# Kernel optimization log

Hardware: AMD Instinct MI355X
Metric: run time of the kernel (lower is better)

The kernel has to match this reference:

```python
import jax, jax.numpy as jnp
import numpy as np

N = 65536          # total nodes across batch
C = 256            # in channels
COUT = 256         # out channels
B = 8              # batch size (graphs)
EMB = 512          # emb channels
N_EDGE_TYPE = 7
N_NODE_TYPE = 7
AVG_DEGREE = 7
E = N * AVG_DEGREE
GROUP = 32         # min(32, channels)
EPS = 1e-5


def setup_inputs() -> dict:
    key = jax.random.key(0)
    ks = jax.random.split(key, 10)
    # GraphConv init: uniform xavier-like with fan scaled by avg_degree
    std = (2.0 / float(AVG_DEGREE * C + AVG_DEGREE * COUT)) ** 0.5
    a = (3.0 ** 0.5) * std
    return {
        "x": jax.random.normal(ks[0], (N, C), jnp.float32),
        "emb": jax.random.normal(ks[1], (B, EMB), jnp.float32),
        "batch_id": jnp.sort(jax.random.randint(ks[2], (N,), 0, B, jnp.int32)),
        "edge_index": jax.random.randint(ks[3], (2, E), 0, N, jnp.int32),
        "edge_type": jax.random.randint(ks[4], (E,), 0, N_EDGE_TYPE, jnp.int32),
        "node_type": jax.random.randint(ks[5], (N,), 0, N_NODE_TYPE, jnp.int32),
        "gn1_w": jnp.ones((1, C), jnp.float32),
        "gn1_b": jnp.zeros((1, C), jnp.float32),
        "conv1_w": jax.random.uniform(ks[6], (N_EDGE_TYPE * (C + N_NODE_TYPE), COUT), jnp.float32, -a, a),
        "emb_w": jax.random.normal(ks[7], (EMB, COUT), jnp.float32) * 0.02,
        "emb_b": jnp.zeros((COUT,), jnp.float32),
        "gn2_w": jnp.ones((1, COUT), jnp.float32),
        "gn2_b": jnp.zeros((1, COUT), jnp.float32),
        "conv2_w": jax.random.uniform(ks[8], (N_EDGE_TYPE * (COUT + N_NODE_TYPE), COUT), jnp.float32, -a, a),
    }


def _adjust_for_group(t, cpg):
    # sum stats within each group of cpg channels, broadcast back: [B, C]
    if cpg > 1:
        Bsz, Cn = t.shape
        g = Cn // cpg
        t = t.reshape(Bsz, g, cpg).sum(-1, keepdims=True)
        t = jnp.broadcast_to(t, (Bsz, g, cpg)).reshape(Bsz, Cn)
    return t


def dual_octree_group_norm(data, batch_id, w, b):
    # data: [N, C]; per-graph group norm via segment sums
    Cn = data.shape[1]
    cpg = Cn // GROUP
    ones = jnp.ones((data.shape[0], 1), data.dtype)
    count = jax.ops.segment_sum(ones, batch_id, num_segments=B) * cpg   # [B,1]
    inv_count = 1.0 / (count + EPS)
    mean = jax.ops.segment_sum(data, batch_id, num_segments=B) * inv_count
    mean = _adjust_for_group(mean, cpg)
    out = data - mean[batch_id]
    var = jax.ops.segment_sum(out * out, batch_id, num_segments=B) * inv_count
    var = _adjust_for_group(var, cpg)
    inv_std = 1.0 / jnp.sqrt(var + EPS)
    out = out * inv_std[batch_id]
    return out * w + b


def graph_conv(x, weights, edge_index, edge_type, node_type):
    # concat one-hot node type channels
    one_hot = jax.nn.one_hot(node_type, N_NODE_TYPE, dtype=x.dtype)
    xa = jnp.concatenate([x, one_hot], axis=1)          # [N, C+T]
    row, col = edge_index[0], edge_index[1]
    index = row * N_EDGE_TYPE + edge_type               # [E]
    col_data = jax.ops.segment_sum(xa[col], index, num_segments=xa.shape[0] * N_EDGE_TYPE)
    return col_data.reshape(xa.shape[0], -1) @ weights  # [N, COUT]


def reference(x, emb, batch_id, edge_index, edge_type, node_type,
              gn1_w, gn1_b, conv1_w, emb_w, emb_b, gn2_w, gn2_b, conv2_w):
    h = dual_octree_group_norm(x, batch_id, gn1_w, gn1_b)
    h = jax.nn.silu(h)
    h = graph_conv(h, conv1_w, edge_index, edge_type, node_type)
    emb_out = jax.nn.silu(emb) @ emb_w + emb_b          # [B, COUT]
    h = h + emb_out[batch_id]                           # per-batch add (loop in torch)
    h = dual_octree_group_norm(h, batch_id, gn2_w, gn2_b)
    h = jax.nn.silu(h)                                  # dropout p=0 -> identity
    h = graph_conv(h, conv2_w, edge_index, edge_type, node_type)
    return x + h                                        # skip is Identity (Cout==C)
```

## Files before the change

### kernel.cpp

```cpp
#include <hip/hip_runtime.h>
#include <math.h>

#define N_NODES 65536
#define B_GR    8
#define EMB_N   512
#define E_EDGES 458752
#define NSEG    458752
#define TSTRIDE 288
#define GK      2016
#define EPS     1e-5f

typedef unsigned short u16;
typedef unsigned int   u32;
typedef __bf16 bf16x8 __attribute__((ext_vector_type(8)));
typedef float  f32x4  __attribute__((ext_vector_type(4)));
typedef u16    u16x8  __attribute__((ext_vector_type(8)));

__device__ __forceinline__ float bf2f(u16 u) {
    u32 x = ((u32)u) << 16; float f; __builtin_memcpy(&f, &x, 4); return f;
}
__device__ __forceinline__ u16 f2bf(float f) {
    u32 x; __builtin_memcpy(&x, &f, 4);
    u32 r = x + 0x7fffu + ((x >> 16) & 1u);
    return (u16)(r >> 16);
}

#define SW(row, k8) ((k8) ^ (((row) >> 1) & 3))

__global__ __launch_bounds__(256) void zero_kernel(int* __restrict__ hist,
                                                   float* __restrict__ S, float* __restrict__ Q,
                                                   int* __restrict__ cnt) {
    int i = blockIdx.x * 256 + threadIdx.x;
    if (i < NSEG) hist[i] = 0;
    if (i < 2048) { S[i] = 0.f; Q[i] = 0.f; }
    if (i < 8) cnt[i] = 0;
}

__global__ __launch_bounds__(256) void count_kernel(const int* __restrict__ batch_id,
                                                    int* __restrict__ cnt) {
    int i = blockIdx.x * 256 + threadIdx.x;
    int b = batch_id[i];
#pragma unroll
    for (int bb = 0; bb < 8; bb++) {
        unsigned long long m = __ballot(b == bb);
        if ((threadIdx.x & 63) == 0 && m)
            atomicAdd(&cnt[bb], (int)__popcll(m));
    }
}

__global__ __launch_bounds__(256) void prep_kernel(
    const float* __restrict__ w1, const float* __restrict__ w2,
    u16* __restrict__ Wt1, u16* __restrict__ Wt2,
    const float* __restrict__ emb, const float* __restrict__ embw,
    const float* __restrict__ embb, float* __restrict__ embout)
{
    int bid = blockIdx.x, tid = threadIdx.x;
    if (bid < 1008) {
        const float* Win = (bid < 504) ? w1 : w2;
        u16* Wt = (bid < 504) ? Wt1 : Wt2;
        int r  = bid % 504;
        int t  = r / 72;
        int r2 = r % 72;
        int c0 = (r2 / 8) * 32;
        int n0 = (r2 % 8) * 32;
        __shared__ float tile[32][33];
        int cl = tid & 31, rh = tid >> 5;
#pragma unroll
        for (int rr = 0; rr < 4; rr++) {
            int c = c0 + rh + rr * 8;
            float v = 0.f;
            if (c < 263) v = Win[(size_t)(t * 263 + c) * 256 + n0 + cl];
            tile[rh + rr * 8][cl] = v;
        }
        __syncthreads();
#pragma unroll
        for (int rr = 0; rr < 4; rr++) {
            int n = n0 + rh + rr * 8;
            Wt[(size_t)n * GK + t * TSTRIDE + c0 + cl] = f2bf(tile[cl][rh + rr * 8]);
        }
    } else {
        __shared__ float semb[B_GR * EMB_N];
        for (int i = tid; i < B_GR * EMB_N; i += 256) {
            float e = emb[i];
            semb[i] = e / (1.f + expf(-e));
        }
        __syncthreads();
        float acc[8];
        float bb = embb[tid];
#pragma unroll
        for (int b = 0; b < 8; b++) acc[b] = bb;
        for (int k = 0; k < EMB_N; k++) {
            float wv = embw[k * 256 + tid];
#pragma unroll
            for (int b = 0; b < 8; b++) acc[b] += semb[b * EMB_N + k] * wv;
        }
#pragma unroll
        for (int b = 0; b < 8; b++) embout[b * 256 + tid] = acc[b];
    }
}

__global__ __launch_bounds__(256) void stats_kernel(const float* __restrict__ xin,
                                                    const int* __restrict__ batch_id,
                                                    float* __restrict__ S, float* __restrict__ Q) {
    int c = threadIdx.x;
    int n0 = blockIdx.x * 64;
    float s = 0.f, q = 0.f;
    int bcur = batch_id[n0];
    for (int r = 0; r < 64; r++) {
        int n = n0 + r;
        int b = batch_id[n];
        if (b != bcur) {
            atomicAdd(&S[bcur * 256 + c], s);
            atomicAdd(&Q[bcur * 256 + c], q);
            s = 0.f; q = 0.f; bcur = b;
        }
        float v = xin[(size_t)n * 256 + c];
        s += v;
        q = fmaf(v, v, q);
    }
    atomicAdd(&S[bcur * 256 + c], s);
    atomicAdd(&Q[bcur * 256 + c], q);
}

__global__ __launch_bounds__(256) void finalize_kernel(const int* __restrict__ cnt,
                                                       float* __restrict__ S, float* __restrict__ Q,
                                                       float* __restrict__ gmean, float* __restrict__ gistd) {
    int tid = threadIdx.x;
    int b = tid >> 5, g = tid & 31;
    float Sg = 0.f, Qg = 0.f;
#pragma unroll
    for (int k = 0; k < 8; k++) {
        int idx = b * 256 + g * 8 + k;
        Sg += S[idx];
        Qg += Q[idx];
        S[idx] = 0.f;
        Q[idx] = 0.f;
    }
    float cnt8 = (float)cnt[b] * 8.f;
    float D = cnt8 + EPS;
    float m = Sg / D;
    float var = (Qg - 2.f * m * Sg + cnt8 * m * m) / D;
    float istd = rsqrtf(var + EPS);
    gmean[tid] = m;
    gistd[tid] = istd;
}

__global__ __launch_bounds__(256) void norm_silu_kernel(const float* __restrict__ xin,
                                                        const int* __restrict__ batch_id,
                                                        const float* __restrict__ gmean, const float* __restrict__ gistd,
                                                        const float* __restrict__ w, const float* __restrict__ bias,
                                                        u16* __restrict__ yout) {
    int tid = threadIdx.x;
    int n = blockIdx.x * 8 + (tid >> 5);
    int g = tid & 31;
    int c0 = g * 8;
    int b = batch_id[n];
    float m = gmean[b * 32 + g], is = gistd[b * 32 + g];
    u16x8 o;
#pragma unroll
    for (int k = 0; k < 8; k++) {
        float v = (xin[(size_t)n * 256 + c0 + k] - m) * is;
        v = v * w[c0 + k] + bias[c0 + k];
        v = v / (1.f + expf(-v));
        o[k] = f2bf(v);
    }
    *(u16x8*)&yout[(size_t)n * 256 + c0] = o;
}

__global__ __launch_bounds__(256) void hist_kernel(const int* __restrict__ ei, const int* __restrict__ et,
                                                   int* __restrict__ hist) {
    int e = blockIdx.x * 256 + threadIdx.x;
    if (e >= E_EDGES) return;
    int s = ei[e] * 7 + et[e];
    atomicAdd(&hist[s], 1);
}

__global__ __launch_bounds__(512) void scan1_kernel(const int* __restrict__ hist, int* __restrict__ partials) {
    __shared__ int sd[512];
    int i = blockIdx.x * 512 + threadIdx.x;
    sd[threadIdx.x] = hist[i];
    __syncthreads();
    for (int off = 256; off > 0; off >>= 1) {
        if (threadIdx.x < off) sd[threadIdx.x] += sd[threadIdx.x + off];
        __syncthreads();
    }
    if (threadIdx.x == 0) partials[blockIdx.x] = sd[0];
}

__global__ __launch_bounds__(1024) void scan2_kernel(int* __restrict__ partials) {
    __shared__ int sd[1024];
    int t = threadIdx.x;
    int v = (t < 896) ? partials[t] : 0;
    sd[t] = v;
    __syncthreads();
    for (int off = 1; off < 1024; off <<= 1) {
        int u = (t >= off) ? sd[t - off] : 0;
        __syncthreads();
        sd[t] += u;
        __syncthreads();
    }
    if (t < 896) partials[t] = sd[t] - v;
}

__global__ __launch_bounds__(512) void scan3_kernel(int* __restrict__ hist_offs, const int* __restrict__ partials,
                                                    int* __restrict__ cursor) {
    __shared__ int sd[512];
    int t = threadIdx.x;
    int i = blockIdx.x * 512 + t;
    int c = hist_offs[i];
    sd[t] = c;
    __syncthreads();
    for (int off = 1; off < 512; off <<= 1) {
        int u = (t >= off) ? sd[t - off] : 0;
        __syncthreads();
        sd[t] += u;
        __syncthreads();
    }
    int o = partials[blockIdx.x] + sd[t] - c;
    hist_offs[i] = o;
    cursor[i] = o;
}

__global__ __launch_bounds__(256) void fill_kernel(const int* __restrict__ ei, const int* __restrict__ et,
                                                   int* __restrict__ cursor, int* __restrict__ elist) {
    int e = blockIdx.x * 256 + threadIdx.x;
    if (e >= E_EDGES) return;
    int s = ei[e] * 7 + et[e];
    int p = atomicAdd(&cursor[s], 1);
    if (p >= 0 && p < E_EDGES) elist[p] = ei[E_EDGES + e];
}

__global__ __launch_bounds__(512, 4) void gemm_fused_kernel(
    const u16* __restrict__ y, const u16* __restrict__ Bt,
    const int* __restrict__ offs, const int* __restrict__ cursor,
    const int* __restrict__ elist, const int* __restrict__ node_type,
    const int* __restrict__ batch_id, const float* __restrict__ embout,
    const float* __restrict__ xres, float* __restrict__ out, int mode)
{
    __shared__ __align__(16) u16 As[2][64 * 32];
    int tid = threadIdx.x;
    int lane = tid & 63;
    int wn = tid >> 6;
    int lm = lane & 15, lq = lane >> 4;
    int m0 = blockIdx.x * 64;
    int ar = tid >> 3;
    int aq = (tid >> 1) & 3;
    int half = tid & 1;

    f32x4 acc[4][2];
    f32x4 zz = {0.f, 0.f, 0.f, 0.f};
#pragma unroll
    for (int i = 0; i < 4; i++)
#pragma unroll
        for (int j = 0; j < 2; j++) acc[i][j] = zz;

    const u16* btp0 = Bt + (size_t)(wn * 32 + lm) * GK + lq * 8;
    const u16* btp1 = btp0 + (size_t)16 * GK;

    int sbase = (m0 + ar) * 7;
    int st = offs[sbase], en = cursor[sbase];
    int col[2];
    col[0] = (st + half     < en) ? elist[st + half]     : -1;
    col[1] = (st + half + 2 < en) ? elist[st + half + 2] : -1;

    float a8[8];
#pragma unroll
    for (int j = 0; j < 8; j++) a8[j] = 0.f;
#pragma unroll
    for (int u = 0; u < 2; u++)
        if (col[u] >= 0) {
            u16x8 v = *(const u16x8*)&y[(size_t)col[u] * 256 + aq * 8];
#pragma unroll
            for (int j = 0; j < 8; j++) a8[j] += bf2f(v[j]);
        }
    if (en - st > 4)
        for (int e = st + 4 + half; e < en; e += 2) {
            u16x8 v = *(const u16x8*)&y[(size_t)elist[e] * 256 + aq * 8];
#pragma unroll
            for (int j = 0; j < 8; j++) a8[j] += bf2f(v[j]);
        }

    bf16x8 bcur[2], bnxt[2];
    bcur[0] = *(const bf16x8*)&btp0[0];
    bcur[1] = *(const bf16x8*)&btp1[0];

    int st_n = 0, en_n = 0;
    int coln[2] = {-1, -1};
    int buf = 0;

    for (int t = 0; t < 7; t++) {
#pragma unroll
        for (int c9 = 0; c9 < 9; c9++) {
#pragma unroll
            for (int j = 0; j < 8; j++) a8[j] += __shfl_xor(a8[j], 1);
            if (half == 0) {
                u16x8 o;
#pragma unroll
                for (int j = 0; j < 8; j++) o[j] = f2bf(a8[j]);
                *(u16x8*)&As[buf][ar * 32 + SW(ar, aq) * 8] = o;
            }
            __syncthreads();
            bf16x8 a[4];
#pragma unroll
            for (int i = 0; i < 4; i++) {
                int ra = i * 16 + lm;
                a[i] = *(const bf16x8*)&As[buf][ra * 32 + SW(ra, lq) * 8];
            }
            u16x8 gv[2];
            int nt2[2];
#pragma unroll
            for (int j = 0; j < 8; j++) a8[j] = 0.f;
            if (c9 < 7) {
                int cb = (c9 + 1) * 32 + aq * 8;
#pragma unroll
                for (int u = 0; u < 2; u++)
                    if (col[u] >= 0) gv[u] = *(const u16x8*)&y[(size_t)col[u] * 256 + cb];
                int kb = t * TSTRIDE + (c9 + 1) * 32;
                bnxt[0] = *(const bf16x8*)&btp0[kb];
                bnxt[1] = *(const bf16x8*)&btp1[kb];
                if (c9 == 6 && t < 6) {
                    int sn = sbase + t + 1;
                    st_n = offs[sn];
                    en_n = cursor[sn];
                }
            } else if (c9 == 7) {
                if (aq == 0) {
#pragma unroll
                    for (int u = 0; u < 2; u++)
                        nt2[u] = (col[u] >= 0) ? node_type[col[u]] : -1;
                }
                int kb = t * TSTRIDE + 256;
                bnxt[0] = *(const bf16x8*)&btp0[kb];
                bnxt[1] = *(const bf16x8*)&btp1[kb];
                if (t < 6) {
                    coln[0] = (st_n + half     < en_n) ? elist[st_n + half]     : -1;
                    coln[1] = (st_n + half + 2 < en_n) ? elist[st_n + half + 2] : -1;
                }
            } else {
                if (t < 6) {
                    int cb = aq * 8;
#pragma unroll
                    for (int u = 0; u < 2; u++)
                        if (coln[u] >= 0) gv[u] = *(const u16x8*)&y[(size_t)coln[u] * 256 + cb];
                    int kb = (t + 1) * TSTRIDE;
                    bnxt[0] = *(const bf16x8*)&btp0[kb];
                    bnxt[1] = *(const bf16x8*)&btp1[kb];
                }
            }
            __builtin_amdgcn_s_setprio(1);
#pragma unroll
            for (int i = 0; i < 4; i++)
#pragma unroll
                for (int j = 0; j < 2; j++)
                    acc[i][j] = __builtin_amdgcn_mfma_f32_16x16x32_bf16(a[i], bcur[j], acc[i][j], 0, 0, 0);
            __builtin_amdgcn_s_setprio(0);
            if (c9 < 7) {
#pragma unroll
                for (int u = 0; u < 2; u++)
                    if (col[u] >= 0) {
#pragma unroll
                        for (int j = 0; j < 8; j++) a8[j] += bf2f(gv[u][j]);
                    }
                if (en - st > 4) {
                    int cb = (c9 + 1) * 32 + aq * 8;
                    for (int e = st + 4 + half; e < en; e += 2) {
                        u16x8 v = *(const u16x8*)&y[(size_t)elist[e] * 256 + cb];
#pragma unroll
                        for (int j = 0; j < 8; j++) a8[j] += bf2f(v[j]);
                    }
                }
            } else if (c9 == 7) {
                if (aq == 0) {
#pragma unroll
                    for (int u = 0; u < 2; u++)
                        if (col[u] >= 0) {
#pragma unroll
                            for (int j = 0; j < 7; j++) a8[j] += (nt2[u] == j) ? 1.f : 0.f;
                        }
                    if (en - st > 4)
                        for (int e = st + 4 + half; e < en; e += 2) {
                            int nt = node_type[elist[e]];
#pragma unroll
                            for (int j = 0; j < 7; j++) a8[j] += (nt == j) ? 1.f : 0.f;
                        }
                }
            } else {
                if (t < 6) {
#pragma unroll
                    for (int u = 0; u < 2; u++)
                        if (coln[u] >= 0) {
#pragma unroll
                            for (int j = 0; j < 8; j++) a8[j] += bf2f(gv[u][j]);
                        }
                    if (en_n - st_n > 4)
                        for (int e = st_n + 4 + half; e < en_n; e += 2) {
                            u16x8 v = *(const u16x8*)&y[(size_t)elist[e] * 256 + aq * 8];
#pragma unroll
                            for (int j = 0; j < 8; j++) a8[j] += bf2f(v[j]);
                        }
                    col[0] = coln[0]; col[1] = coln[1];
                    st = st_n; en = en_n;
                }
            }
            bcur[0] = bnxt[0]; bcur[1] = bnxt[1];
            buf ^= 1;
        }
    }

#pragma unroll
    for (int i = 0; i < 4; i++) {
#pragma unroll
        for (int r = 0; r < 4; r++) {
            size_t m = (size_t)m0 + i * 16 + lq * 4 + r;
            float addv[2];
            if (mode == 0) {
                int b = batch_id[m];
#pragma unroll
                for (int j = 0; j < 2; j++) addv[j] = embout[b * 256 + wn * 32 + j * 16 + lm];
            } else {
#pragma unroll
                for (int j = 0; j < 2; j++) addv[j] = xres[m * 256 + wn * 32 + j * 16 + lm];
            }
#pragma unroll
            for (int j = 0; j < 2; j++) {
                int n = wn * 32 + j * 16 + lm;
                out[m * 256 + n] = acc[i][j][r] + addv[j];
            }
        }
    }
}

extern "C" void kernel_launch(void* const* d_in, const int* in_sizes, int n_in,
                              void* d_out, int out_size, void* d_ws, size_t ws_size,
                              hipStream_t stream) {
    const float* x    = (const float*)d_in[0];
    const float* emb  = (const float*)d_in[1];
    const int* bid    = (const int*)d_in[2];
    const int* ei     = (const int*)d_in[3];
    const int* et     = (const int*)d_in[4];
    const int* ntp    = (const int*)d_in[5];
    const float* gn1w = (const float*)d_in[6];
    const float* gn1b = (const float*)d_in[7];
    const float* w1   = (const float*)d_in[8];
    const float* embw = (const float*)d_in[9];
    const float* embb = (const float*)d_in[10];
    const float* gn2w = (const float*)d_in[11];
    const float* gn2b = (const float*)d_in[12];
    const float* w2   = (const float*)d_in[13];
    float* out = (float*)d_out;

    char* p = (char*)d_ws;
    size_t off = 0;
    auto nxt = [&](size_t bytes) -> void* {
        void* r = p + off;
        off += (bytes + 255) & ~(size_t)255;
        return r;
    };
    u16*   y       = (u16*)nxt((size_t)N_NODES * 256 * 2);
    u16*   Wt1     = (u16*)nxt((size_t)256 * GK * 2);
    u16*   Wt2     = (u16*)nxt((size_t)256 * GK * 2);
    float* embout  = (float*)nxt(8 * 256 * 4);
    float* S       = (float*)nxt(2048 * 4);
    float* Q       = (float*)nxt(2048 * 4);
    float* gmean   = (float*)nxt(256 * 4);
    float* gistd   = (float*)nxt(256 * 4);
    int*   cnt     = (int*)nxt(8 * 4);
    int*   offs    = (int*)nxt((size_t)NSEG * 4);
    int*   cursor  = (int*)nxt((size_t)NSEG * 4);
    int*   parts   = (int*)nxt(1024 * 4);
    int*   elist   = (int*)nxt((size_t)E_EDGES * 4);
    float* h2      = out;
    (void)ws_size; (void)in_sizes; (void)n_in; (void)out_size;

    zero_kernel<<<1792, 256, 0, stream>>>(offs, S, Q, cnt);
    count_kernel<<<256, 256, 0, stream>>>(bid, cnt);
    prep_kernel<<<1009, 256, 0, stream>>>(w1, w2, Wt1, Wt2, emb, embw, embb, embout);
    stats_kernel<<<1024, 256, 0, stream>>>(x, bid, S, Q);
    finalize_kernel<<<1, 256, 0, stream>>>(cnt, S, Q, gmean, gistd);
    norm_silu_kernel<<<8192, 256, 0, stream>>>(x, bid, gmean, gistd, gn1w, gn1b, y);
    hist_kernel<<<1792, 256, 0, stream>>>(ei, et, offs);
    scan1_kernel<<<896, 512, 0, stream>>>(offs, parts);
    scan2_kernel<<<1, 1024, 0, stream>>>(parts);
    scan3_kernel<<<896, 512, 0, stream>>>(offs, parts, cursor);
    fill_kernel<<<1792, 256, 0, stream>>>(ei, et, cursor, elist);
    gemm_fused_kernel<<<1024, 512, 0, stream>>>(y, Wt1, offs, cursor, elist, ntp, bid, embout, x, h2, 0);
    stats_kernel<<<1024, 256, 0, stream>>>(h2, bid, S, Q);
    finalize_kernel<<<1, 256, 0, stream>>>(cnt, S, Q, gmean, gistd);
    norm_silu_kernel<<<8192, 256, 0, stream>>>(h2, bid, gmean, gistd, gn2w, gn2b, y);
    gemm_fused_kernel<<<1024, 512, 0, stream>>>(y, Wt2, offs, cursor, elist, ntp, bid, embout, x, out, 1);
}
```

Baseline: 720.1 us.

## Fuse prep kernels, inline group-norm finalize, and restructure gather-GEMM A staging

Merges the count, weight-transpose, embedding and first stats passes into one front kernel, and runs histogram and norm blocks in a single launch. Each norm block now computes group mean/istd itself, which removes the finalize kernels. Zeroing moves to memsets plus a tail of the fill kernel. The fused GEMM now gathers a whole 256-channel neighbour row per edge type into a wide padded LDS tile with a 3-deep B register prefetch, instead of a per-32-chunk double buffer. This cuts launches and repeated gather index work, at the cost of more registers and LDS, which may lower occupancy.

```diff
diff --git a/kernel.cpp b/kernel.cpp
--- a/kernel.cpp
+++ b/kernel.cpp
@@ -8,6 +8,7 @@
 #define NSEG    458752
 #define TSTRIDE 288
 #define GK      2016
+#define ASTRIDE 296
 #define EPS     1e-5f
 
 typedef unsigned short u16;
@@ -25,85 +26,11 @@
     return (u16)(r >> 16);
 }
 
-#define SW(row, k8) ((k8) ^ (((row) >> 1) & 3))
-
-__global__ __launch_bounds__(256) void zero_kernel(int* __restrict__ hist,
-                                                   float* __restrict__ S, float* __restrict__ Q,
-                                                   int* __restrict__ cnt) {
-    int i = blockIdx.x * 256 + threadIdx.x;
-    if (i < NSEG) hist[i] = 0;
-    if (i < 2048) { S[i] = 0.f; Q[i] = 0.f; }
-    if (i < 8) cnt[i] = 0;
-}
-
-__global__ __launch_bounds__(256) void count_kernel(const int* __restrict__ batch_id,
-                                                    int* __restrict__ cnt) {
-    int i = blockIdx.x * 256 + threadIdx.x;
-    int b = batch_id[i];
-#pragma unroll
-    for (int bb = 0; bb < 8; bb++) {
-        unsigned long long m = __ballot(b == bb);
-        if ((threadIdx.x & 63) == 0 && m)
-            atomicAdd(&cnt[bb], (int)__popcll(m));
-    }
-}
-
-__global__ __launch_bounds__(256) void prep_kernel(
-    const float* __restrict__ w1, const float* __restrict__ w2,
-    u16* __restrict__ Wt1, u16* __restrict__ Wt2,
-    const float* __restrict__ emb, const float* __restrict__ embw,
-    const float* __restrict__ embb, float* __restrict__ embout)
-{
-    int bid = blockIdx.x, tid = threadIdx.x;
-    if (bid < 1008) {
-        const float* Win = (bid < 504) ? w1 : w2;
-        u16* Wt = (bid < 504) ? Wt1 : Wt2;
-        int r  = bid % 504;
-        int t  = r / 72;
-        int r2 = r % 72;
-        int c0 = (r2 / 8) * 32;
-        int n0 = (r2 % 8) * 32;
-        __shared__ float tile[32][33];
-        int cl = tid & 31, rh = tid >> 5;
-#pragma unroll
-        for (int rr = 0; rr < 4; rr++) {
-            int c = c0 + rh + rr * 8;
-            float v = 0.f;
-            if (c < 263) v = Win[(size_t)(t * 263 + c) * 256 + n0 + cl];
-            tile[rh + rr * 8][cl] = v;
-        }
-        __syncthreads();
-#pragma unroll
-        for (int rr = 0; rr < 4; rr++) {
-            int n = n0 + rh + rr * 8;
-            Wt[(size_t)n * GK + t * TSTRIDE + c0 + cl] = f2bf(tile[cl][rh + rr * 8]);
-        }
-    } else {
-        __shared__ float semb[B_GR * EMB_N];
-        for (int i = tid; i < B_GR * EMB_N; i += 256) {
-            float e = emb[i];
-            semb[i] = e / (1.f + expf(-e));
-        }
-        __syncthreads();
-        float acc[8];
-        float bb = embb[tid];
-#pragma unroll
-        for (int b = 0; b < 8; b++) acc[b] = bb;
-        for (int k = 0; k < EMB_N; k++) {
-            float wv = embw[k * 256 + tid];
-#pragma unroll
-            for (int b = 0; b < 8; b++) acc[b] += semb[b * EMB_N + k] * wv;
-        }
-#pragma unroll
-        for (int b = 0; b < 8; b++) embout[b * 256 + tid] = acc[b];
-    }
-}
-
-__global__ __launch_bounds__(256) void stats_kernel(const float* __restrict__ xin,
-                                                    const int* __restrict__ batch_id,
-                                                    float* __restrict__ S, float* __restrict__ Q) {
-    int c = threadIdx.x;
-    int n0 = blockIdx.x * 64;
+__device__ __forceinline__ void stats_body(int nb, int tid, const float* __restrict__ xin,
+                                           const int* __restrict__ batch_id,
+                                           float* __restrict__ S, float* __restrict__ Q) {
+    int c = tid;
+    int n0 = nb * 64;
     float s = 0.f, q = 0.f;
     int bcur = batch_id[n0];
     for (int r = 0; r < 64; r++) {
@@ -122,57 +49,137 @@
     atomicAdd(&Q[bcur * 256 + c], q);
 }
 
-__global__ __launch_bounds__(256) void finalize_kernel(const int* __restrict__ cnt,
-                                                       float* __restrict__ S, float* __restrict__ Q,
-                                                       float* __restrict__ gmean, float* __restrict__ gistd) {
-    int tid = threadIdx.x;
-    int b = tid >> 5, g = tid & 31;
-    float Sg = 0.f, Qg = 0.f;
-#pragma unroll
-    for (int k = 0; k < 8; k++) {
-        int idx = b * 256 + g * 8 + k;
-        Sg += S[idx];
-        Qg += Q[idx];
-        S[idx] = 0.f;
-        Q[idx] = 0.f;
-    }
-    float cnt8 = (float)cnt[b] * 8.f;
-    float D = cnt8 + EPS;
-    float m = Sg / D;
-    float var = (Qg - 2.f * m * Sg + cnt8 * m * m) / D;
-    float istd = rsqrtf(var + EPS);
-    gmean[tid] = m;
-    gistd[tid] = istd;
-}
-
-__global__ __launch_bounds__(256) void norm_silu_kernel(const float* __restrict__ xin,
-                                                        const int* __restrict__ batch_id,
-                                                        const float* __restrict__ gmean, const float* __restrict__ gistd,
-                                                        const float* __restrict__ w, const float* __restrict__ bias,
-                                                        u16* __restrict__ yout) {
-    int tid = threadIdx.x;
-    int n = blockIdx.x * 8 + (tid >> 5);
+__device__ __forceinline__ void norm_body(int nb, int tid, const float* __restrict__ xin,
+                                          const int* __restrict__ batch_id,
+                                          const float* __restrict__ S, const float* __restrict__ Q,
+                                          const int* __restrict__ cnt,
+                                          const float* __restrict__ w, const float* __restrict__ bias,
+                                          u16* __restrict__ yout) {
+    __shared__ float smean[256], sistd[256];
+    {
+        int b = tid >> 5, g = tid & 31;
+        float Sg = 0.f, Qg = 0.f;
+#pragma unroll
+        for (int k = 0; k < 8; k++) {
+            Sg += S[b * 256 + g * 8 + k];
+            Qg += Q[b * 256 + g * 8 + k];
+        }
+        float cnt8 = (float)cnt[b] * 8.f;
+        float D = cnt8 + EPS;
+        float m = Sg / D;
+        float var = (Qg - 2.f * m * Sg + cnt8 * m * m) / D;
+        smean[tid] = m;
+        sistd[tid] = rsqrtf(var + EPS);
+    }
+    __syncthreads();
+    int n = nb * 8 + (tid >> 5);
     int g = tid & 31;
     int c0 = g * 8;
     int b = batch_id[n];
-    float m = gmean[b * 32 + g], is = gistd[b * 32 + g];
+    float m = smean[b * 32 + g], is = sistd[b * 32 + g];
     u16x8 o;
 #pragma unroll
     for (int k = 0; k < 8; k++) {
         float v = (xin[(size_t)n * 256 + c0 + k] - m) * is;
         v = v * w[c0 + k] + bias[c0 + k];
-        v = v / (1.f + expf(-v));
+        v = v / (1.f + __expf(-v));
         o[k] = f2bf(v);
     }
     *(u16x8*)&yout[(size_t)n * 256 + c0] = o;
 }
 
-__global__ __launch_bounds__(256) void hist_kernel(const int* __restrict__ ei, const int* __restrict__ et,
-                                                   int* __restrict__ hist) {
-    int e = blockIdx.x * 256 + threadIdx.x;
-    if (e >= E_EDGES) return;
-    int s = ei[e] * 7 + et[e];
-    atomicAdd(&hist[s], 1);
+__global__ __launch_bounds__(256) void front_kernel(
+    const int* __restrict__ batch_id, int* __restrict__ cnt,
+    const float* __restrict__ w1, const float* __restrict__ w2,
+    u16* __restrict__ Wt1, u16* __restrict__ Wt2,
+    const float* __restrict__ emb, const float* __restrict__ embw,
+    const float* __restrict__ embb, float* __restrict__ embout,
+    const float* __restrict__ x, float* __restrict__ S, float* __restrict__ Q)
+{
+    int bid = blockIdx.x, tid = threadIdx.x;
+    if (bid < 256) {
+        int i = bid * 256 + tid;
+        int b = batch_id[i];
+#pragma unroll
+        for (int bb = 0; bb < 8; bb++) {
+            unsigned long long mm = __ballot(b == bb);
+            if ((tid & 63) == 0 && mm) atomicAdd(&cnt[bb], (int)__popcll(mm));
+        }
+    } else if (bid < 1264) {
+        int r = bid - 256;
+        const float* Win = (r < 504) ? w1 : w2;
+        u16* Wt = (r < 504) ? Wt1 : Wt2;
+        r %= 504;
+        int t  = r / 72;
+        int r2 = r % 72;
+        int cc0 = (r2 / 8) * 32;
+        int n0  = (r2 % 8) * 32;
+        __shared__ float tile[32][33];
+        int cl = tid & 31, rh = tid >> 5;
+#pragma unroll
+        for (int rr = 0; rr < 4; rr++) {
+            int c = cc0 + rh + rr * 8;
+            float v = 0.f;
+            if (c < 263) v = Win[(size_t)(t * 263 + c) * 256 + n0 + cl];
+            tile[rh + rr * 8][cl] = v;
+        }
+        __syncthreads();
+#pragma unroll
+        for (int rr = 0; rr < 4; rr++) {
+            int n = n0 + rh + rr * 8;
+            Wt[(size_t)n * GK + t * TSTRIDE + cc0 + cl] = f2bf(tile[cl][rh + rr * 8]);
+        }
+    } else if (bid == 1264) {
+        __shared__ float semb[B_GR * EMB_N];
+        for (int i = tid; i < B_GR * EMB_N; i += 256) {
+            float e = emb[i];
+            semb[i] = e / (1.f + __expf(-e));
+        }
+        __syncthreads();
+        float acc[8];
+        float bb = embb[tid];
+#pragma unroll
+        for (int b = 0; b < 8; b++) acc[b] = bb;
+        for (int k = 0; k < EMB_N; k++) {
+            float wv = embw[k * 256 + tid];
+#pragma unroll
+            for (int b = 0; b < 8; b++) acc[b] += semb[b * EMB_N + k] * wv;
+        }
+#pragma unroll
+        for (int b = 0; b < 8; b++) embout[b * 256 + tid] = acc[b];
+    } else {
+        stats_body(bid - 1265, tid, x, batch_id, S, Q);
+    }
+}
+
+__global__ __launch_bounds__(256) void hist_norm_kernel(
+    const int* __restrict__ ei, const int* __restrict__ et, int* __restrict__ hist,
+    const float* __restrict__ xin, const int* __restrict__ batch_id,
+    const float* __restrict__ S, const float* __restrict__ Q, const int* __restrict__ cnt,
+    const float* __restrict__ w, const float* __restrict__ bias, u16* __restrict__ yout)
+{
+    int bid = blockIdx.x;
+    if (bid < 1792) {
+        int e = bid * 256 + threadIdx.x;
+        int s = ei[e] * 7 + et[e];
+        atomicAdd(&hist[s], 1);
+    } else {
+        norm_body(bid - 1792, threadIdx.x, xin, batch_id, S, Q, cnt, w, bias, yout);
+    }
+}
+
+__global__ __launch_bounds__(256) void stats_kernel(const float* __restrict__ xin,
+                                                    const int* __restrict__ batch_id,
+                                                    float* __restrict__ S, float* __restrict__ Q) {
+    stats_body(blockIdx.x, threadIdx.x, xin, batch_id, S, Q);
+}
+__global__ __launch_bounds__(256) void norm_kernel(const float* __restrict__ xin,
+                                                   const int* __restrict__ batch_id,
+                                                   const float* __restrict__ S, const float* __restrict__ Q,
+                                                   const int* __restrict__ cnt,
+                                                   const float* __restrict__ w, const float* __restrict__ bias,
+                                                   u16* __restrict__ yout) {
+    norm_body(blockIdx.x, threadIdx.x, xin, batch_id, S, Q, cnt, w, bias, yout);
 }
 
 __global__ __launch_bounds__(512) void scan1_kernel(const int* __restrict__ hist, int* __restrict__ partials) {
@@ -221,13 +228,19 @@
     cursor[i] = o;
 }
 
-__global__ __launch_bounds__(256) void fill_kernel(const int* __restrict__ ei, const int* __restrict__ et,
-                                                   int* __restrict__ cursor, int* __restrict__ elist) {
-    int e = blockIdx.x * 256 + threadIdx.x;
-    if (e >= E_EDGES) return;
-    int s = ei[e] * 7 + et[e];
-    int p = atomicAdd(&cursor[s], 1);
-    if (p >= 0 && p < E_EDGES) elist[p] = ei[E_EDGES + e];
+__global__ __launch_bounds__(256) void fill_zero_kernel(const int* __restrict__ ei, const int* __restrict__ et,
+                                                        int* __restrict__ cursor, int* __restrict__ elist,
+                                                        float* __restrict__ S, float* __restrict__ Q) {
+    int bid = blockIdx.x;
+    if (bid < 1792) {
+        int e = bid * 256 + threadIdx.x;
+        int s = ei[e] * 7 + et[e];
+        int p = atomicAdd(&cursor[s], 1);
+        if (p >= 0 && p < E_EDGES) elist[p] = ei[E_EDGES + e];
+    } else {
+        int i = (bid - 1792) * 256 + threadIdx.x;
+        S[i] = 0.f; Q[i] = 0.f;
+    }
 }
 
 __global__ __launch_bounds__(512, 4) void gemm_fused_kernel(
@@ -237,15 +250,15 @@
     const int* __restrict__ batch_id, const float* __restrict__ embout,
     const float* __restrict__ xres, float* __restrict__ out, int mode)
 {
-    __shared__ __align__(16) u16 As[2][64 * 32];
+    __shared__ __align__(16) u16 As[64 * ASTRIDE];
     int tid = threadIdx.x;
     int lane = tid & 63;
     int wn = tid >> 6;
     int lm = lane & 15, lq = lane >> 4;
     int m0 = blockIdx.x * 64;
     int ar = tid >> 3;
-    int aq = (tid >> 1) & 3;
-    int half = tid & 1;
+    int tq = tid & 7;
+    const size_t yq = (size_t)tq * 32;
 
     f32x4 acc[4][2];
     f32x4 zz = {0.f, 0.f, 0.f, 0.f};
@@ -258,153 +271,163 @@
     const u16* btp1 = btp0 + (size_t)16 * GK;
 
     int sbase = (m0 + ar) * 7;
+
     int st = offs[sbase], en = cursor[sbase];
-    int col[2];
-    col[0] = (st + half     < en) ? elist[st + half]     : -1;
-    col[1] = (st + half + 2 < en) ? elist[st + half + 2] : -1;
-
-    float a8[8];
-#pragma unroll
-    for (int j = 0; j < 8; j++) a8[j] = 0.f;
-#pragma unroll
-    for (int u = 0; u < 2; u++)
-        if (col[u] >= 0) {
-            u16x8 v = *(const u16x8*)&y[(size_t)col[u] * 256 + aq * 8];
-#pragma unroll
-            for (int j = 0; j < 8; j++) a8[j] += bf2f(v[j]);
-        }
-    if (en - st > 4)
-        for (int e = st + 4 + half; e < en; e += 2) {
-            u16x8 v = *(const u16x8*)&y[(size_t)elist[e] * 256 + aq * 8];
-#pragma unroll
-            for (int j = 0; j < 8; j++) a8[j] += bf2f(v[j]);
-        }
-
-    bf16x8 bcur[2], bnxt[2];
-    bcur[0] = *(const bf16x8*)&btp0[0];
-    bcur[1] = *(const bf16x8*)&btp1[0];
-
-    int st_n = 0, en_n = 0;
-    int coln[2] = {-1, -1};
-    int buf = 0;
+    int c0 = (st     < en) ? elist[st]     : -1;
+    int c1 = (st + 1 < en) ? elist[st + 1] : -1;
+    int c2 = (st + 2 < en) ? elist[st + 2] : -1;
+    int c3 = (st + 3 < en) ? elist[st + 3] : -1;
+    int nt0 = -1, nt1 = -1;
+    u16x8 e0[4], e1[4];
+    if (c0 >= 0) {
+#pragma unroll
+        for (int q = 0; q < 4; q++) e0[q] = *(const u16x8*)&y[(size_t)c0 * 256 + yq + q * 8];
+    }
+    if (c1 >= 0) {
+#pragma unroll
+        for (int q = 0; q < 4; q++) e1[q] = *(const u16x8*)&y[(size_t)c1 * 256 + yq + q * 8];
+    }
+    if (tq == 0) {
+        if (c0 >= 0) nt0 = node_type[c0];
+        if (c1 >= 0) nt1 = node_type[c1];
+    }
+    bf16x8 bR[3][2];
+#pragma unroll
+    for (int p = 0; p < 3; p++) {
+        bR[p][0] = *(const bf16x8*)&btp0[p * 32];
+        bR[p][1] = *(const bf16x8*)&btp1[p * 32];
+    }
+
+    int stn = 0, enn = 0, c0n = -1, c1n = -1, c2n = -1, c3n = -1, nt0n = -1, nt1n = -1;
 
     for (int t = 0; t < 7; t++) {
+        int cnt = en - st;
+        u16x8 x2[4], x3[4];
+        int nt2 = -1, nt3 = -1;
+        if (c2 >= 0) {
+#pragma unroll
+            for (int q = 0; q < 4; q++) x2[q] = *(const u16x8*)&y[(size_t)c2 * 256 + yq + q * 8];
+            if (tq == 0) nt2 = node_type[c2];
+        }
+        if (c3 >= 0) {
+#pragma unroll
+            for (int q = 0; q < 4; q++) x3[q] = *(const u16x8*)&y[(size_t)c3 * 256 + yq + q * 8];
+            if (tq == 0) nt3 = node_type[c3];
+        }
+        float s[4][8];
+#pragma unroll
+        for (int q = 0; q < 4; q++)
+#pragma unroll
+            for (int j = 0; j < 8; j++) {
+                float v = 0.f;
+                if (c0 >= 0) v += bf2f(e0[q][j]);
+                if (c1 >= 0) v += bf2f(e1[q][j]);
+                s[q][j] = v;
+            }
+        if (c2 >= 0) {
+#pragma unroll
+            for (int q = 0; q < 4; q++)
+#pragma unroll
+                for (int j = 0; j < 8; j++) s[q][j] += bf2f(x2[q][j]);
+        }
+        if (c3 >= 0) {
+#pragma unroll
+            for (int q = 0; q < 4; q++)
+#pragma unroll
+                for (int j = 0; j < 8; j++) s[q][j] += bf2f(x3[q][j]);
+        }
+        float oh[7];
+        if (tq == 0) {
+#pragma unroll
+            for (int j = 0; j < 7; j++)
+                oh[j] = (nt0 == j ? 1.f : 0.f) + (nt1 == j ? 1.f : 0.f)
+                      + (nt2 == j ? 1.f : 0.f) + (nt3 == j ? 1.f : 0.f);
+        }
+        if (cnt > 4) {
+            for (int e = st + 4; e < en; e++) {
+                int c = elist[e];
+                u16x8 r[4];
+#pragma unroll
+                for (int q = 0; q < 4; q++) r[q] = *(const u16x8*)&y[(size_t)c * 256 + yq + q * 8];
+#pragma unroll
+                for (int q = 0; q < 4; q++)
+#pragma unroll
+                    for (int j = 0; j < 8; j++) s[q][j] += bf2f(r[q][j]);
+                if (tq == 0) {
+                    int nt = node_type[c];
+#pragma unroll
+                    for (int j = 0; j < 7; j++) oh[j] += (nt == j) ? 1.f : 0.f;
+                }
+            }
+        }
+        __syncthreads();
+#pragma unroll
+        for (int q = 0; q < 4; q++) {
+            u16x8 w;
+#pragma unroll
+            for (int j = 0; j < 8; j++) w[j] = f2bf(s[q][j]);
+            *(u16x8*)&As[ar * ASTRIDE + tq * 32 + q * 8] = w;
+        }
+        if (tq == 0) {
+            u16x8 w, z;
+#pragma unroll
+            for (int j = 0; j < 8; j++) { w[j] = 0; z[j] = 0; }
+#pragma unroll
+            for (int j = 0; j < 7; j++) w[j] = f2bf(oh[j]);
+            *(u16x8*)&As[ar * ASTRIDE + 256] = w;
+            *(u16x8*)&As[ar * ASTRIDE + 264] = z;
+            *(u16x8*)&As[ar * ASTRIDE + 272] = z;
+            *(u16x8*)&As[ar * ASTRIDE + 280] = z;
+        }
+        __syncthreads();
 #pragma unroll
         for (int c9 = 0; c9 < 9; c9++) {
-#pragma unroll
-            for (int j = 0; j < 8; j++) a8[j] += __shfl_xor(a8[j], 1);
-            if (half == 0) {
-                u16x8 o;
-#pragma unroll
-                for (int j = 0; j < 8; j++) o[j] = f2bf(a8[j]);
-                *(u16x8*)&As[buf][ar * 32 + SW(ar, aq) * 8] = o;
-            }
-            __syncthreads();
             bf16x8 a[4];
 #pragma unroll
-            for (int i = 0; i < 4; i++) {
-                int ra = i * 16 + lm;
-                a[i] = *(const bf16x8*)&As[buf][ra * 32 + SW(ra, lq) * 8];
-            }
-            u16x8 gv[2];
-            int nt2[2];
-#pragma unroll
-            for (int j = 0; j < 8; j++) a8[j] = 0.f;
-            if (c9 < 7) {
-                int cb = (c9 + 1) * 32 + aq * 8;
-#pragma unroll
-                for (int u = 0; u < 2; u++)
-                    if (col[u] >= 0) gv[u] = *(const u16x8*)&y[(size_t)col[u] * 256 + cb];
-                int kb = t * TSTRIDE + (c9 + 1) * 32;
-                bnxt[0] = *(const bf16x8*)&btp0[kb];
-                bnxt[1] = *(const bf16x8*)&btp1[kb];
-                if (c9 == 6 && t < 6) {
-                    int sn = sbase + t + 1;
-                    st_n = offs[sn];
-                    en_n = cursor[sn];
+            for (int i = 0; i < 4; i++)
+                a[i] = *(const bf16x8*)&As[(i * 16 + lm) * ASTRIDE + c9 * 32 + lq * 8];
+            bf16x8 bn0, bn1;
+            const bool doB = (t < 6) || (c9 < 6);
+            if (doB) {
+                int kb = t * TSTRIDE + (c9 + 3) * 32;
+                bn0 = *(const bf16x8*)&btp0[kb];
+                bn1 = *(const bf16x8*)&btp1[kb];
+            }
+            if (t < 6) {
+                if (c9 == 0) { stn = offs[sbase + t + 1]; enn = cursor[sbase + t + 1]; }
+                if (c9 == 2) {
+                    c0n = (stn     < enn) ? elist[stn]     : -1;
+                    c1n = (stn + 1 < enn) ? elist[stn + 1] : -1;
+                    c2n = (stn + 2 < enn) ? elist[stn + 2] : -1;
+                    c3n = (stn + 3 < enn) ? elist[stn + 3] : -1;
                 }
-            } else if (c9 == 7) {
-                if (aq == 0) {
-#pragma unroll
-                    for (int u = 0; u < 2; u++)
-                        nt2[u] = (col[u] >= 0) ? node_type[col[u]] : -1;
-                }
-                int kb = t * TSTRIDE + 256;
-                bnxt[0] = *(const bf16x8*)&btp0[kb];
-                bnxt[1] = *(const bf16x8*)&btp1[kb];
-                if (t < 6) {
-                    coln[0] = (st_n + half     < en_n) ? elist[st_n + half]     : -1;
-                    coln[1] = (st_n + half + 2 < en_n) ? elist[st_n + half + 2] : -1;
-                }
-            } else {
-                if (t < 6) {
-                    int cb = aq * 8;
-#pragma unroll
-                    for (int u = 0; u < 2; u++)
-                        if (coln[u] >= 0) gv[u] = *(const u16x8*)&y[(size_t)coln[u] * 256 + cb];
-                    int kb = (t + 1) * TSTRIDE;
-                    bnxt[0] = *(const bf16x8*)&btp0[kb];
-                    bnxt[1] = *(const bf16x8*)&btp1[kb];
-                }
-            }
-            __builtin_amdgcn_s_setprio(1);
-#pragma unroll
-            for (int i = 0; i < 4; i++)
-#pragma unroll
-                for (int j = 0; j < 2; j++)
-                    acc[i][j] = __builtin_amdgcn_mfma_f32_16x16x32_bf16(a[i], bcur[j], acc[i][j], 0, 0, 0);
-            __builtin_amdgcn_s_setprio(0);
-            if (c9 < 7) {
-#pragma unroll
-                for (int u = 0; u < 2; u++)
-                    if (col[u] >= 0) {
-#pragma unroll
-                        for (int j = 0; j < 8; j++) a8[j] += bf2f(gv[u][j]);
+                if (c9 == 5) {
+                    if (c0n >= 0) {
+#pragma unroll
+                        for (int q = 0; q < 4; q++) e0[q] = *(const u16x8*)&y[(size_t)c0n * 256 + yq + q * 8];
                     }
-                if (en - st > 4) {
-                    int cb = (c9 + 1) * 32 + aq * 8;
-                    for (int e = st + 4 + half; e < en; e += 2) {
-                        u16x8 v = *(const u16x8*)&y[(size_t)elist[e] * 256 + cb];
-#pragma unroll
-                        for (int j = 0; j < 8; j++) a8[j] += bf2f(v[j]);
+                    if (c1n >= 0) {
+#pragma unroll
+                        for (int q = 0; q < 4; q++) e1[q] = *(const u16x8*)&y[(size_t)c1n * 256 + yq + q * 8];
+                    }
+                    if (tq == 0) {
+                        nt0n = (c0n >= 0) ? node_type[c0n] : -1;
+                        nt1n = (c1n >= 0) ? node_type[c1n] : -1;
                     }
                 }
-            } else if (c9 == 7) {
-                if (aq == 0) {
-#pragma unroll
-                    for (int u = 0; u < 2; u++)
-                        if (col[u] >= 0) {
-#pragma unroll
-                            for (int j = 0; j < 7; j++) a8[j] += (nt2[u] == j) ? 1.f : 0.f;
-                        }
-                    if (en - st > 4)
-                        for (int e = st + 4 + half; e < en; e += 2) {
-                            int nt = node_type[elist[e]];
-#pragma unroll
-                            for (int j = 0; j < 7; j++) a8[j] += (nt == j) ? 1.f : 0.f;
-                        }
-                }
-            } else {
-                if (t < 6) {
-#pragma unroll
-                    for (int u = 0; u < 2; u++)
-                        if (coln[u] >= 0) {
-#pragma unroll
-                            for (int j = 0; j < 8; j++) a8[j] += bf2f(gv[u][j]);
-                        }
-                    if (en_n - st_n > 4)
-                        for (int e = st_n + 4 + half; e < en_n; e += 2) {
-                            u16x8 v = *(const u16x8*)&y[(size_t)elist[e] * 256 + aq * 8];
-#pragma unroll
-                            for (int j = 0; j < 8; j++) a8[j] += bf2f(v[j]);
-                        }
-                    col[0] = coln[0]; col[1] = coln[1];
-                    st = st_n; en = en_n;
-                }
-            }
-            bcur[0] = bnxt[0]; bcur[1] = bnxt[1];
-            buf ^= 1;
-        }
+            }
+            __builtin_amdgcn_s_setprio(1);
+#pragma unroll
+            for (int i = 0; i < 4; i++) {
+                acc[i][0] = __builtin_amdgcn_mfma_f32_16x16x32_bf16(a[i], bR[c9 % 3][0], acc[i][0], 0, 0, 0);
+                acc[i][1] = __builtin_amdgcn_mfma_f32_16x16x32_bf16(a[i], bR[c9 % 3][1], acc[i][1], 0, 0, 0);
+            }
+            __builtin_amdgcn_s_setprio(0);
+            if (doB) { bR[c9 % 3][0] = bn0; bR[c9 % 3][1] = bn1; }
+        }
+        st = stn; en = enn;
+        c0 = c0n; c1 = c1n; c2 = c2n; c3 = c3n;
+        nt0 = nt0n; nt1 = nt1n;
     }
 
 #pragma unroll
@@ -462,8 +485,6 @@
     float* embout  = (float*)nxt(8 * 256 * 4);
     float* S       = (float*)nxt(2048 * 4);
     float* Q       = (float*)nxt(2048 * 4);
-    float* gmean   = (float*)nxt(256 * 4);
-    float* gistd   = (float*)nxt(256 * 4);
     int*   cnt     = (int*)nxt(8 * 4);
     int*   offs    = (int*)nxt((size_t)NSEG * 4);
     int*   cursor  = (int*)nxt((size_t)NSEG * 4);
@@ -472,20 +493,17 @@
     float* h2      = out;
     (void)ws_size; (void)in_sizes; (void)n_in; (void)out_size;
 
-    zero_kernel<<<1792, 256, 0, stream>>>(offs, S, Q, cnt);
-    count_kernel<<<256, 256, 0, stream>>>(bid, cnt);
-    prep_kernel<<<1009, 256, 0, stream>>>(w1, w2, Wt1, Wt2, emb, embw, embb, embout);
-    stats_kernel<<<1024, 256, 0, stream>>>(x, bid, S, Q);
-    finalize_kernel<<<1, 256, 0, stream>>>(cnt, S, Q, gmean, gistd);
-    norm_silu_kernel<<<8192, 256, 0, stream>>>(x, bid, gmean, gistd, gn1w, gn1b, y);
-    hist_kernel<<<1792, 256, 0, stream>>>(ei, et, offs);
+    hipMemsetAsync(offs, 0, (size_t)NSEG * 4, stream);
+    hipMemsetAsync(S, 0, 8192 + 8192 + 256, stream);
+    front_kernel<<<2289, 256, 0, stream>>>(bid, cnt, w1, w2, Wt1, Wt2,
+                                           emb, embw, embb, embout, x, S, Q);
+    hist_norm_kernel<<<9984, 256, 0, stream>>>(ei, et, offs, x, bid, S, Q, cnt, gn1w, gn1b, y);
     scan1_kernel<<<896, 512, 0, stream>>>(offs, parts);
     scan2_kernel<<<1, 1024, 0, stream>>>(parts);
     scan3_kernel<<<896, 512, 0, stream>>>(offs, parts, cursor);
-    fill_kernel<<<1792, 256, 0, stream>>>(ei, et, cursor, elist);
+    fill_zero_kernel<<<1800, 256, 0, stream>>>(ei, et, cursor, elist, S, Q);
     gemm_fused_kernel<<<1024, 512, 0, stream>>>(y, Wt1, offs, cursor, elist, ntp, bid, embout, x, h2, 0);
     stats_kernel<<<1024, 256, 0, stream>>>(h2, bid, S, Q);
-    finalize_kernel<<<1, 256, 0, stream>>>(cnt, S, Q, gmean, gistd);
-    norm_silu_kernel<<<8192, 256, 0, stream>>>(h2, bid, gmean, gistd, gn2w, gn2b, y);
+    norm_kernel<<<8192, 256, 0, stream>>>(h2, bid, S, Q, cnt, gn2w, gn2b, y);
     gemm_fused_kernel<<<1024, 512, 0, stream>>>(y, Wt2, offs, cursor, elist, ntp, bid, embout, x, out, 1);
 }
```

Result: slower. 1.140 ms (+58.3%).
